# Performance work log

Measured on AMD Instinct MI355X. Metric: run time of the kernel, lower is better.

The kernel has to match this reference:

```python
import jax, jax.numpy as jnp
import numpy as np

B, H, N, D = 1, 8, 2048, 64  # n >> d: fastmax's intended long-seq / small-head-dim regime


def setup_inputs() -> dict:
    key = jax.random.key(0)
    kq, kk, kv, kr = jax.random.split(key, 4)
    q = jax.random.normal(kq, (B, H, N, D), dtype=jnp.float32)
    k = jax.random.normal(kk, (B, H, N, D), dtype=jnp.float32)
    v = jax.random.normal(kv, (B, H, N, D), dtype=jnp.float32)
    rpe_matrix = jax.random.normal(kr, (2 * N - 1, D), dtype=jnp.float32)
    return {"q": q, "k": k, "v": v, "rpe_matrix": rpe_matrix, "mask": 1}


def reference(q, k, v, rpe_matrix, mask):
    # Fastmax: 2nd-order Taylor approximation of softmax attention,
    # weight(i,j) = 1 + s_ij + s_ij^2 / 2 where s_ij = q_i . (k_j) + q_i . rpe[i-j+n-1],
    # normalized by the row-sum, optionally causal (mask).
    b, h, n, d = q.shape
    # content scores: (b,h,n,n)
    s = jnp.einsum('bhid,bhjd->bhij', q, k)
    # RPE scores: project q onto every relative-position embedding, then gather
    # the (i,j) -> i-j+n-1 diagonal structure.  qr: (b,h,n,2n-1)
    qr = jnp.einsum('bhid,md->bhim', q, rpe_matrix)
    i = jnp.arange(n)[:, None]
    j = jnp.arange(n)[None, :]
    rel = i - j + (n - 1)  # (n,n) in [0, 2n-2]
    s = s + jnp.take_along_axis(qr, rel[None, None], axis=-1)
    # Taylor-2 exp approximation
    w = 1.0 + s + 0.5 * s * s
    if mask:  # causal
        w = jnp.where(j <= i, w, 0.0)
    denom = jnp.sum(w, axis=-1, keepdims=True)  # (b,h,n,1)
    out = jnp.einsum('bhij,bhjd->bhid', w, v) / denom
    return out
```

## Files before the change

kernel.cpp:

```cpp
#include <hip/hip_runtime.h>
#include <hip/hip_bf16.h>

#define HH 8
#define NN 2048
#define DD 64

typedef __attribute__((ext_vector_type(8))) short bf16x8;
typedef __attribute__((ext_vector_type(4))) float f32x4;
typedef __attribute__((ext_vector_type(8))) unsigned short u16x8;
typedef unsigned short ushort_t;

static __device__ __forceinline__ unsigned short f2bf(float x) {
    union { float f; unsigned u; } un; un.f = x;
    unsigned r = un.u + 0x7FFFu + ((un.u >> 16) & 1u);
    return (unsigned short)(r >> 16);
}
static __device__ __forceinline__ float bf2f(unsigned short u) {
    union { unsigned u; float f; } un; un.u = ((unsigned)u) << 16;
    return un.f;
}

#define OFF_Q  0u
#define OFF_K  2097152u
#define OFF_VT 4194304u
#define OFF_R  6291456u
#define OFF_P  6815744u
#define WS_NEED (OFF_P + 256u*3u*2u*32u*68u*4u)

#define NQ4 262144
#define NR4 65520
#define CVT_BLOCKS 2305
__global__ void pre_kernel(const float* __restrict__ q, const float* __restrict__ k,
                           const float* __restrict__ r, const float* __restrict__ v,
                           ushort_t* __restrict__ ws) {
    __shared__ __align__(16) ushort_t T[64][72];
    if (blockIdx.x < CVT_BLOCKS) {
        int idx = blockIdx.x * 256 + threadIdx.x;
        const float* src; ushort_t* dst; int off;
        if (idx < NQ4) { src = q; dst = (ushort_t*)((char*)ws + OFF_Q); off = idx; }
        else if (idx < 2 * NQ4) { src = k; dst = (ushort_t*)((char*)ws + OFF_K); off = idx - NQ4; }
        else if (idx < 2 * NQ4 + NR4) { src = r; dst = (ushort_t*)((char*)ws + OFF_R); off = idx - 2 * NQ4; }
        else return;
        float4 f = *(const float4*)&src[4 * (size_t)off];
        ushort4 u; u.x = f2bf(f.x); u.y = f2bf(f.y); u.z = f2bf(f.z); u.w = f2bf(f.w);
        *(ushort4*)&dst[4 * (size_t)off] = u;
    } else {
        ushort_t* vt = (ushort_t*)((char*)ws + OFF_VT);
        const int bb = blockIdx.x - CVT_BLOCKS;
        const int h = bb >> 5;
        const int n0 = (bb & 31) * 64;
        const int tid = threadIdx.x;
        const float* vh = v + (size_t)h * NN * DD;
        #pragma unroll
        for (int p = 0; p < 4; ++p) {
            int c = tid + 256 * p; int rr = c >> 4, dc = (c & 15) << 2;
            float4 f = *(const float4*)&vh[(size_t)(n0 + rr) * DD + dc];
            T[dc + 0][rr] = f2bf(f.x); T[dc + 1][rr] = f2bf(f.y);
            T[dc + 2][rr] = f2bf(f.z); T[dc + 3][rr] = f2bf(f.w);
        }
        __syncthreads();
        #pragma unroll
        for (int p = 0; p < 2; ++p) {
            int c = tid + 256 * p; int d = c >> 3, nn = (c & 7) << 3;
            *(u16x8*)&vt[((size_t)h * 64 + d) * NN + n0 + nn] = *(const u16x8*)&T[d][nn];
        }
    }
}

__global__ __launch_bounds__(256, 3)
void fastmax_main(const ushort_t* __restrict__ wsb, float* __restrict__ wsPart)
{
    __shared__ __align__(16) ushort_t Qs[32][72];
    __shared__ __align__(16) ushort_t Ks[64][72];
    __shared__ __align__(16) ushort_t Bs[96][72];
    __shared__ __align__(16) ushort_t Vts[80][72];
    __shared__ __align__(16) unsigned char U[11776];

    ushort_t* TsP = (ushort_t*)U;
    ushort_t* WsP = (ushort_t*)(U + 6656);
    float*    Epi = (float*)U;

    const ushort_t* qb  = (const ushort_t*)((const char*)wsb + OFF_Q);
    const ushort_t* kb  = (const ushort_t*)((const char*)wsb + OFF_K);
    const ushort_t* vtb = (const ushort_t*)((const char*)wsb + OFF_VT);
    const ushort_t* rb  = (const ushort_t*)((const char*)wsb + OFF_R);

    const int tid = threadIdx.x;
    const int w   = tid >> 6;
    const int l   = tid & 63;
    const int lq  = l >> 4;
    const int ln  = l & 15;
    const int rt  = w & 1;
    const int ch  = w >> 1;

    const int stream = blockIdx.x;
    const int sub    = blockIdx.y;
    const int head   = stream & 7;
    const int p      = stream >> 3;
    const int tileA  = 63 - p;
    const int njtA   = (tileA >> 1) + 1;
    const int tileB  = p;
    const int njtB   = (p >> 1) + 1;
    const int u0     = 11 * sub, u1 = u0 + 11;

    const ushort_t* qh  = qb  + (size_t)head * NN * DD;
    const ushort_t* kh  = kb  + (size_t)head * NN * DD;
    const ushort_t* vth = vtb + (size_t)head * DD * NN;

    for (int idx = tid; idx < 16 * 72; idx += 256) {
        int r = idx / 72, c = idx - r * 72;
        Vts[64 + r][c] = (r == 0) ? (ushort_t)0x3F80 : (ushort_t)0;
    }

    const int sw = 16 * rt - 32 * ch + 32;

    #pragma unroll 1
    for (int seg = 0; seg < 2; ++seg) {
        int tile, jlo, jhi, role;
        if (seg == 0) {
            tile = tileB; role = 0;
            jlo = u0; jhi = (u1 < njtB) ? u1 : njtB;
        } else {
            tile = tileA; role = 1;
            int a0 = (u0 > njtB) ? u0 : njtB;
            jlo = a0 - njtB; jhi = u1 - njtB;
            if (jhi > njtA) jhi = njtA;
        }
        if (jlo >= jhi) continue;
        const int i0 = tile * 32;

        __syncthreads();
        { int r = tid >> 3, dc = (tid & 7) << 3;
          *(u16x8*)&Qs[r][dc] = *(const u16x8*)&qh[(size_t)(i0 + r) * DD + dc]; }
        __syncthreads();

        bf16x8 qf0 = *(const bf16x8*)&Qs[16 * rt + ln][ 0 + 8 * lq];
        bf16x8 qf1 = *(const bf16x8*)&Qs[16 * rt + ln][32 + 8 * lq];
        bf16x8 vdf = *(const bf16x8*)&Vts[64 + ln][32 * ch + 8 * lq];

        f32x4 acc0 = {0,0,0,0}, acc1 = {0,0,0,0}, acc2 = {0,0,0,0}, acc3 = {0,0,0,0};
        f32x4 accD = {0,0,0,0};

        for (int jt = jlo; jt < jhi; ++jt) {
            const int j0 = jt * 64;
            __syncthreads();

            #pragma unroll
            for (int p2 = 0; p2 < 2; ++p2) {
                int c = tid + 256 * p2; int r = c >> 3, dc = (c & 7) << 3;
                *(u16x8*)&Ks[r][dc] = *(const u16x8*)&kh[(size_t)(j0 + r) * DD + dc];
            }
            const int relbase = i0 - j0 + 1984;
            #pragma unroll
            for (int p2 = 0; p2 < 3; ++p2) {
                int c = tid + 256 * p2; int r = c >> 3, dc = (c & 7) << 3;
                int row = relbase + r; if (row > 4094) row = 4094;
                *(u16x8*)&Bs[r][dc] = *(const u16x8*)&rb[(size_t)row * DD + dc];
            }
            #pragma unroll
            for (int p2 = 0; p2 < 2; ++p2) {
                int c = tid + 256 * p2; int d = c >> 3, nc = (c & 7) << 3;
                *(u16x8*)&Vts[d][nc] = *(const u16x8*)&vth[(size_t)d * NN + j0 + nc];
            }
            __syncthreads();

            f32x4 s0 = {0,0,0,0}, s1 = {0,0,0,0};
            {
                bf16x8 b00 = *(const bf16x8*)&Ks[32 * ch      + ln][ 0 + 8 * lq];
                bf16x8 b01 = *(const bf16x8*)&Ks[32 * ch      + ln][32 + 8 * lq];
                bf16x8 b10 = *(const bf16x8*)&Ks[32 * ch + 16 + ln][ 0 + 8 * lq];
                bf16x8 b11 = *(const bf16x8*)&Ks[32 * ch + 16 + ln][32 + 8 * lq];
                s0 = __builtin_amdgcn_mfma_f32_16x16x32_bf16(qf0, b00, s0, 0, 0, 0);
                s0 = __builtin_amdgcn_mfma_f32_16x16x32_bf16(qf1, b01, s0, 0, 0, 0);
                s1 = __builtin_amdgcn_mfma_f32_16x16x32_bf16(qf0, b10, s1, 0, 0, 0);
                s1 = __builtin_amdgcn_mfma_f32_16x16x32_bf16(qf1, b11, s1, 0, 0, 0);
            }

            #pragma unroll
            for (int bt = 0; bt < 3; ++bt) {
                f32x4 t = {0,0,0,0};
                bf16x8 b0 = *(const bf16x8*)&Bs[sw + 16 * bt + ln][ 0 + 8 * lq];
                bf16x8 b1 = *(const bf16x8*)&Bs[sw + 16 * bt + ln][32 + 8 * lq];
                t = __builtin_amdgcn_mfma_f32_16x16x32_bf16(qf0, b0, t, 0, 0, 0);
                t = __builtin_amdgcn_mfma_f32_16x16x32_bf16(qf1, b1, t, 0, 0, 0);
                #pragma unroll
                for (int e = 0; e < 4; ++e)
                    TsP[(w * 16 + 4 * lq + e) * 52 + 16 * bt + ln] = f2bf(t[e]);
            }

            #pragma unroll
            for (int ct = 0; ct < 2; ++ct) {
                f32x4 sv = ct ? s1 : s0;
                #pragma unroll
                for (int e = 0; e < 4; ++e) {
                    int rp = 4 * lq + e;
                    int cp = 16 * ct + ln;
                    int bw = rp - cp + 31;
                    float s = sv[e] + bf2f(TsP[(w * 16 + rp) * 52 + bw]);
                    float wv = 1.0f + s + 0.5f * s * s;
                    if (j0 + 32 * ch + cp > i0 + 16 * rt + rp) wv = 0.0f;
                    WsP[(w * 16 + rp) * 40 + cp] = f2bf(wv);
                }
            }

            {
                bf16x8 af = *(const bf16x8*)&WsP[(w * 16 + ln) * 40 + 8 * lq];
                bf16x8 b;
                b = *(const bf16x8*)&Vts[ 0 + ln][32 * ch + 8 * lq];
                acc0 = __builtin_amdgcn_mfma_f32_16x16x32_bf16(af, b, acc0, 0, 0, 0);
                b = *(const bf16x8*)&Vts[16 + ln][32 * ch + 8 * lq];
                acc1 = __builtin_amdgcn_mfma_f32_16x16x32_bf16(af, b, acc1, 0, 0, 0);
                b = *(const bf16x8*)&Vts[32 + ln][32 * ch + 8 * lq];
                acc2 = __builtin_amdgcn_mfma_f32_16x16x32_bf16(af, b, acc2, 0, 0, 0);
                b = *(const bf16x8*)&Vts[48 + ln][32 * ch + 8 * lq];
                acc3 = __builtin_amdgcn_mfma_f32_16x16x32_bf16(af, b, acc3, 0, 0, 0);
                accD = __builtin_amdgcn_mfma_f32_16x16x32_bf16(af, vdf, accD, 0, 0, 0);
            }
        }

        __syncthreads();
        if (ch == 0) {
            #pragma unroll
            for (int e = 0; e < 4; ++e) {
                int r = 16 * rt + 4 * lq + e;
                Epi[r * 68 +  0 + ln] = acc0[e];
                Epi[r * 68 + 16 + ln] = acc1[e];
                Epi[r * 68 + 32 + ln] = acc2[e];
                Epi[r * 68 + 48 + ln] = acc3[e];
                if (ln == 0) Epi[r * 68 + 64] = accD[e];
            }
        }
        __syncthreads();
        if (ch == 1) {
            #pragma unroll
            for (int e = 0; e < 4; ++e) {
                int r = 16 * rt + 4 * lq + e;
                Epi[r * 68 +  0 + ln] += acc0[e];
                Epi[r * 68 + 16 + ln] += acc1[e];
                Epi[r * 68 + 32 + ln] += acc2[e];
                Epi[r * 68 + 48 + ln] += acc3[e];
                if (ln == 0) Epi[r * 68 + 64] += accD[e];
            }
        }
        __syncthreads();
        {
            float* dst = wsPart + ((size_t)((stream * 3 + sub) * 2 + role)) * (32 * 68);
            for (int idx = tid; idx < 32 * 68; idx += 256) dst[idx] = Epi[idx];
        }
    }
}

__global__ void combine_kernel(const float* __restrict__ wsPart, float* __restrict__ outg) {
    const int c = blockIdx.x;
    const int head = c >> 6;
    const int t = c & 63;
    const int p = (t < 63 - t) ? t : 63 - t;
    const int role = (t == p) ? 0 : 1;
    const int stream = p * 8 + head;
    const int njtB = (p >> 1) + 1;
    const float* P[3]; int nP = 0;
    #pragma unroll
    for (int s = 0; s < 3; ++s) {
        bool valid = role ? (11 * s + 11 > njtB) : (11 * s < njtB);
        if (valid) P[nP++] = wsPart + ((size_t)((stream * 3 + s) * 2 + role)) * (32 * 68);
    }
    float* oh = outg + (size_t)head * NN * DD;
    #pragma unroll
    for (int e2 = 0; e2 < 8; ++e2) {
        int idx = threadIdx.x + 256 * e2;
        int r = idx >> 6, d = idx & 63;
        float num = 0.f, den = 0.f;
        for (int s = 0; s < nP; ++s) {
            num += P[s][r * 68 + d];
            den += P[s][r * 68 + 64];
        }
        oh[(size_t)(t * 32 + r) * DD + d] = num / den;
    }
}

__global__ __launch_bounds__(256, 2)
void fastmax_fallback(const float* __restrict__ qg0, const float* __restrict__ kg0,
                      const float* __restrict__ vg0, const float* __restrict__ rg,
                      float* __restrict__ outg)
{
    __shared__ __align__(16) ushort_t Qs[32][72];
    __shared__ __align__(16) ushort_t Ks[64][72];
    __shared__ __align__(16) ushort_t Bs[96][72];
    __shared__ __align__(16) ushort_t Vts[96][72];
    __shared__ __align__(16) float    Tsf[32][97];
    __shared__ __align__(16) ushort_t Wsf[32][72];
    __shared__ float denomLds[32];

    const int tid = threadIdx.x;
    const int w = tid >> 6, l = tid & 63, lq = l >> 4, ln = l & 15;
    const int head = blockIdx.x & 7, ib = blockIdx.x >> 3;
    const int it = 63 - ib, i0 = it * 32, njt = (it >> 1) + 1;
    const float* qg = qg0 + (size_t)head * NN * DD;
    const float* kg = kg0 + (size_t)head * NN * DD;
    const float* vg = vg0 + (size_t)head * NN * DD;
    float* og = outg + (size_t)head * NN * DD;
    {
        #pragma unroll
        for (int p = 0; p < 2; ++p) {
            int c = tid + 256 * p; int r = c >> 4, dc = (c & 15) << 2;
            float4 f = *(const float4*)&qg[(size_t)(i0 + r) * DD + dc];
            ushort4 u; u.x = f2bf(f.x); u.y = f2bf(f.y); u.z = f2bf(f.z); u.w = f2bf(f.w);
            *(ushort4*)&Qs[r][dc] = u;
        }
        for (int idx = tid; idx < 32 * 72; idx += 256) {
            int rr = idx / 72, cc = idx - rr * 72;
            Vts[64 + rr][cc] = (rr == 0) ? (ushort_t)0x3F80 : (ushort_t)0;
        }
    }
    f32x4 a0 = {0,0,0,0}, a1 = {0,0,0,0}, a2 = {0,0,0,0};
    const int pr = w & 1, rt = w & 1, cp = w >> 1;
    for (int jt = 0; jt < njt; ++jt) {
        const int j0 = jt * 64;
        __syncthreads();
        #pragma unroll
        for (int p = 0; p < 4; ++p) {
            int c = tid + 256 * p; int r = c >> 4, dc = (c & 15) << 2;
            float4 f = *(const float4*)&kg[(size_t)(j0 + r) * DD + dc];
            ushort4 u; u.x = f2bf(f.x); u.y = f2bf(f.y); u.z = f2bf(f.z); u.w = f2bf(f.w);
            *(ushort4*)&Ks[r][dc] = u;
        }
        const int relbase = i0 - j0 + 1984;
        #pragma unroll
        for (int p = 0; p < 6; ++p) {
            int c = tid + 256 * p; int r = c >> 4, dc = (c & 15) << 2;
            int row = relbase + r; if (row > 4094) row = 4094;
            float4 f = *(const float4*)&rg[(size_t)row * DD + dc];
            ushort4 u; u.x = f2bf(f.x); u.y = f2bf(f.y); u.z = f2bf(f.z); u.w = f2bf(f.w);
            *(ushort4*)&Bs[r][dc] = u;
        }
        #pragma unroll
        for (int p = 0; p < 4; ++p) {
            int c = tid + 256 * p; int r = c >> 4, dc = (c & 15) << 2;
            float4 f = *(const float4*)&vg[(size_t)(j0 + r) * DD + dc];
            Vts[dc + 0][r] = f2bf(f.x); Vts[dc + 1][r] = f2bf(f.y);
            Vts[dc + 2][r] = f2bf(f.z); Vts[dc + 3][r] = f2bf(f.w);
        }
        __syncthreads();
        f32x4 s0 = {0,0,0,0}, s1 = {0,0,0,0};
        #pragma unroll
        for (int ks = 0; ks < 2; ++ks) {
            bf16x8 a = *(const bf16x8*)&Qs[16 * rt + ln][32 * ks + 8 * lq];
            bf16x8 b0 = *(const bf16x8*)&Ks[32 * cp + ln][32 * ks + 8 * lq];
            bf16x8 b1 = *(const bf16x8*)&Ks[32 * cp + 16 + ln][32 * ks + 8 * lq];
            s0 = __builtin_amdgcn_mfma_f32_16x16x32_bf16(a, b0, s0, 0, 0, 0);
            s1 = __builtin_amdgcn_mfma_f32_16x16x32_bf16(a, b1, s1, 0, 0, 0);
        }
        #pragma unroll
        for (int kk = 0; kk < 3; ++kk) {
            int bt = (w >> 1) + 2 * kk;
            f32x4 t = {0,0,0,0};
            #pragma unroll
            for (int ks = 0; ks < 2; ++ks) {
                bf16x8 a = *(const bf16x8*)&Qs[16 * rt + ln][32 * ks + 8 * lq];
                bf16x8 b = *(const bf16x8*)&Bs[16 * bt + ln][32 * ks + 8 * lq];
                t = __builtin_amdgcn_mfma_f32_16x16x32_bf16(a, b, t, 0, 0, 0);
            }
            #pragma unroll
            for (int e = 0; e < 4; ++e) Tsf[16 * rt + 4 * lq + e][16 * bt + ln] = t[e];
        }
        __syncthreads();
        #pragma unroll
        for (int ct2 = 0; ct2 < 2; ++ct2) {
            f32x4 sv = ct2 ? s1 : s0;
            int c_loc = 32 * cp + 16 * ct2 + ln, j = j0 + c_loc;
            #pragma unroll
            for (int e = 0; e < 4; ++e) {
                int r_loc = 16 * rt + 4 * lq + e, i = i0 + r_loc;
                float s = sv[e] + Tsf[r_loc][r_loc - c_loc + 63];
                float wv = 1.0f + s + 0.5f * s * s;
                if (j > i) wv = 0.0f;
                Wsf[r_loc][c_loc] = f2bf(wv);
            }
        }
        __syncthreads();
        {
            bf16x8 af0 = *(const bf16x8*)&Wsf[16 * pr + ln][ 0 + 8 * lq];
            bf16x8 af1 = *(const bf16x8*)&Wsf[16 * pr + ln][32 + 8 * lq];
            int pn0 = w >> 1; bf16x8 b;
            b = *(const bf16x8*)&Vts[16 * (pn0 + 0) + ln][ 0 + 8 * lq];
            a0 = __builtin_amdgcn_mfma_f32_16x16x32_bf16(af0, b, a0, 0, 0, 0);
            b = *(const bf16x8*)&Vts[16 * (pn0 + 0) + ln][32 + 8 * lq];
            a0 = __builtin_amdgcn_mfma_f32_16x16x32_bf16(af1, b, a0, 0, 0, 0);
            b = *(const bf16x8*)&Vts[16 * (pn0 + 2) + ln][ 0 + 8 * lq];
            a1 = __builtin_amdgcn_mfma_f32_16x16x32_bf16(af0, b, a1, 0, 0, 0);
            b = *(const bf16x8*)&Vts[16 * (pn0 + 2) + ln][32 + 8 * lq];
            a1 = __builtin_amdgcn_mfma_f32_16x16x32_bf16(af1, b, a1, 0, 0, 0);
            b = *(const bf16x8*)&Vts[16 * (pn0 + 4) + ln][ 0 + 8 * lq];
            a2 = __builtin_amdgcn_mfma_f32_16x16x32_bf16(af0, b, a2, 0, 0, 0);
            b = *(const bf16x8*)&Vts[16 * (pn0 + 4) + ln][32 + 8 * lq];
            a2 = __builtin_amdgcn_mfma_f32_16x16x32_bf16(af1, b, a2, 0, 0, 0);
        }
    }
    if (w < 2 && ln == 0) {
        #pragma unroll
        for (int e = 0; e < 4; ++e) denomLds[16 * pr + 4 * lq + e] = a2[e];
    }
    __syncthreads();
    #pragma unroll
    for (int k = 0; k < 2; ++k) {
        int pn = (w >> 1) + 2 * k;
        f32x4 acc = k ? a1 : a0;
        #pragma unroll
        for (int e = 0; e < 4; ++e) {
            int r_loc = 16 * pr + 4 * lq + e;
            og[(size_t)(i0 + r_loc) * DD + 16 * pn + ln] = acc[e] / denomLds[r_loc];
        }
    }
}

extern "C" void kernel_launch(void* const* d_in, const int* in_sizes, int n_in,
                              void* d_out, int out_size, void* d_ws, size_t ws_size,
                              hipStream_t stream) {
    const float* q   = (const float*)d_in[0];
    const float* k   = (const float*)d_in[1];
    const float* v   = (const float*)d_in[2];
    const float* rpe = (const float*)d_in[3];
    float* out = (float*)d_out;

    if (ws_size >= WS_NEED) {
        ushort_t* wsb = (ushort_t*)d_ws;
        float* wsPart = (float*)((char*)d_ws + OFF_P);
        hipLaunchKernelGGL(pre_kernel, dim3(CVT_BLOCKS + 256), dim3(256), 0, stream,
                           q, k, rpe, v, wsb);
        hipLaunchKernelGGL(fastmax_main, dim3(256, 3), dim3(256), 0, stream, wsb, wsPart);
        hipLaunchKernelGGL(combine_kernel, dim3(512), dim3(256), 0, stream, wsPart, out);
    } else {
        hipLaunchKernelGGL(fastmax_fallback, dim3(512), dim3(256), 0, stream,
                           q, k, v, rpe, out);
    }
}
```

Before: 111.8 us.

## Restructure main kernel into independent per-wave 32x32 MFMA tasks without LDS staging

Each wave now independently handles one 32-row query tile over a slice of key tiles, giving 1536 wave tasks split six ways per stream instead of three. It switches from 16x16x32 to 32x32x16 MFMA and reads K, RPE and V^T fragments directly from global memory instead of staging them through shared LDS tiles with block-wide barriers. LDS is used only per wave for the RPE diagonal gather and the weight matrix. The aim is to remove __syncthreads overhead and raise parallelism, at the cost of more global/L2 traffic, more partial results for the combine kernel to read, and larger register accumulators.

```diff
diff --git a/kernel.cpp b/kernel.cpp
--- a/kernel.cpp
+++ b/kernel.cpp
@@ -6,7 +6,7 @@
 #define DD 64
 
 typedef __attribute__((ext_vector_type(8))) short bf16x8;
-typedef __attribute__((ext_vector_type(4))) float f32x4;
+typedef __attribute__((ext_vector_type(16))) float f32x16;
 typedef __attribute__((ext_vector_type(8))) unsigned short u16x8;
 typedef unsigned short ushort_t;
 
@@ -14,10 +14,6 @@
     union { float f; unsigned u; } un; un.f = x;
     unsigned r = un.u + 0x7FFFu + ((un.u >> 16) & 1u);
     return (unsigned short)(r >> 16);
-}
-static __device__ __forceinline__ float bf2f(unsigned short u) {
-    union { unsigned u; float f; } un; un.u = ((unsigned)u) << 16;
-    return un.f;
 }
 
 #define OFF_Q  0u
@@ -25,7 +21,7 @@
 #define OFF_VT 4194304u
 #define OFF_R  6291456u
 #define OFF_P  6815744u
-#define WS_NEED (OFF_P + 256u*3u*2u*32u*68u*4u)
+#define WS_NEED (OFF_P + 1536u*2u*2080u*4u)
 
 #define NQ4 262144
 #define NR4 65520
@@ -67,18 +63,11 @@
     }
 }
 
-__global__ __launch_bounds__(256, 3)
+__global__ __launch_bounds__(128, 2)
 void fastmax_main(const ushort_t* __restrict__ wsb, float* __restrict__ wsPart)
 {
-    __shared__ __align__(16) ushort_t Qs[32][72];
-    __shared__ __align__(16) ushort_t Ks[64][72];
-    __shared__ __align__(16) ushort_t Bs[96][72];
-    __shared__ __align__(16) ushort_t Vts[80][72];
-    __shared__ __align__(16) unsigned char U[11776];
-
-    ushort_t* TsP = (ushort_t*)U;
-    ushort_t* WsP = (ushort_t*)(U + 6656);
-    float*    Epi = (float*)U;
+    __shared__ __align__(16) float    Ts[2][96 * 34];
+    __shared__ __align__(16) ushort_t Ws[2][32 * 96];
 
     const ushort_t* qb  = (const ushort_t*)((const char*)wsb + OFF_Q);
     const ushort_t* kb  = (const ushort_t*)((const char*)wsb + OFF_K);
@@ -86,183 +75,152 @@
     const ushort_t* rb  = (const ushort_t*)((const char*)wsb + OFF_R);
 
     const int tid = threadIdx.x;
-    const int w   = tid >> 6;
+    const int wv  = tid >> 6;
     const int l   = tid & 63;
-    const int lq  = l >> 4;
-    const int ln  = l & 15;
-    const int rt  = w & 1;
-    const int ch  = w >> 1;
-
-    const int stream = blockIdx.x;
-    const int sub    = blockIdx.y;
-    const int head   = stream & 7;
-    const int p      = stream >> 3;
-    const int tileA  = 63 - p;
-    const int njtA   = (tileA >> 1) + 1;
-    const int tileB  = p;
-    const int njtB   = (p >> 1) + 1;
-    const int u0     = 11 * sub, u1 = u0 + 11;
+    const int ln  = l & 31;
+    const int h2  = l >> 5;
+    float*    tsW = &Ts[wv][0];
+    ushort_t* wsW = &Ws[wv][0];
+
+    const int wtask = blockIdx.x * 2 + wv;
+    const int s     = wtask / 6;
+    const int c     = wtask - 6 * s;
+    const int head  = s & 7;
+    const int p     = s >> 3;
+    const int u0    = (33 * c + 5) / 6;
+    const int u1    = (33 * c + 38) / 6;
+    const int njtB  = (p >> 1) + 1;
 
     const ushort_t* qh  = qb  + (size_t)head * NN * DD;
     const ushort_t* kh  = kb  + (size_t)head * NN * DD;
     const ushort_t* vth = vtb + (size_t)head * DD * NN;
 
-    for (int idx = tid; idx < 16 * 72; idx += 256) {
-        int r = idx / 72, c = idx - r * 72;
-        Vts[64 + r][c] = (r == 0) ? (ushort_t)0x3F80 : (ushort_t)0;
-    }
-
-    const int sw = 16 * rt - 32 * ch + 32;
+    const short one = (ln == 0) ? (short)0x3F80 : (short)0;
+    const bf16x8 dfrag = {one, one, one, one, one, one, one, one};
 
     #pragma unroll 1
-    for (int seg = 0; seg < 2; ++seg) {
-        int tile, jlo, jhi, role;
-        if (seg == 0) {
-            tile = tileB; role = 0;
-            jlo = u0; jhi = (u1 < njtB) ? u1 : njtB;
-        } else {
-            tile = tileA; role = 1;
-            int a0 = (u0 > njtB) ? u0 : njtB;
-            jlo = a0 - njtB; jhi = u1 - njtB;
-            if (jhi > njtA) jhi = njtA;
-        }
+    for (int role = 0; role < 2; ++role) {
+        const int tile = role ? (63 - p) : p;
+        int jlo = role ? ((u0 > njtB ? u0 : njtB) - njtB) : u0;
+        int jhi = role ? (u1 - njtB) : (u1 < njtB ? u1 : njtB);
         if (jlo >= jhi) continue;
         const int i0 = tile * 32;
 
-        __syncthreads();
-        { int r = tid >> 3, dc = (tid & 7) << 3;
-          *(u16x8*)&Qs[r][dc] = *(const u16x8*)&qh[(size_t)(i0 + r) * DD + dc]; }
-        __syncthreads();
-
-        bf16x8 qf0 = *(const bf16x8*)&Qs[16 * rt + ln][ 0 + 8 * lq];
-        bf16x8 qf1 = *(const bf16x8*)&Qs[16 * rt + ln][32 + 8 * lq];
-        bf16x8 vdf = *(const bf16x8*)&Vts[64 + ln][32 * ch + 8 * lq];
-
-        f32x4 acc0 = {0,0,0,0}, acc1 = {0,0,0,0}, acc2 = {0,0,0,0}, acc3 = {0,0,0,0};
-        f32x4 accD = {0,0,0,0};
+        bf16x8 qf0 = *(const bf16x8*)&qh[(i0 + ln) * DD +  0 + 8 * h2];
+        bf16x8 qf1 = *(const bf16x8*)&qh[(i0 + ln) * DD + 16 + 8 * h2];
+        bf16x8 qf2 = *(const bf16x8*)&qh[(i0 + ln) * DD + 32 + 8 * h2];
+        bf16x8 qf3 = *(const bf16x8*)&qh[(i0 + ln) * DD + 48 + 8 * h2];
+
+        f32x16 acc0 = {0,0,0,0,0,0,0,0,0,0,0,0,0,0,0,0};
+        f32x16 acc1 = {0,0,0,0,0,0,0,0,0,0,0,0,0,0,0,0};
+        f32x16 accD = {0,0,0,0,0,0,0,0,0,0,0,0,0,0,0,0};
 
         for (int jt = jlo; jt < jhi; ++jt) {
             const int j0 = jt * 64;
-            __syncthreads();
-
-            #pragma unroll
-            for (int p2 = 0; p2 < 2; ++p2) {
-                int c = tid + 256 * p2; int r = c >> 3, dc = (c & 7) << 3;
-                *(u16x8*)&Ks[r][dc] = *(const u16x8*)&kh[(size_t)(j0 + r) * DD + dc];
-            }
             const int relbase = i0 - j0 + 1984;
-            #pragma unroll
-            for (int p2 = 0; p2 < 3; ++p2) {
-                int c = tid + 256 * p2; int r = c >> 3, dc = (c & 7) << 3;
-                int row = relbase + r; if (row > 4094) row = 4094;
-                *(u16x8*)&Bs[r][dc] = *(const u16x8*)&rb[(size_t)row * DD + dc];
-            }
-            #pragma unroll
-            for (int p2 = 0; p2 < 2; ++p2) {
-                int c = tid + 256 * p2; int d = c >> 3, nc = (c & 7) << 3;
-                *(u16x8*)&Vts[d][nc] = *(const u16x8*)&vth[(size_t)d * NN + j0 + nc];
-            }
-            __syncthreads();
-
-            f32x4 s0 = {0,0,0,0}, s1 = {0,0,0,0};
+
+            f32x16 s0 = {0,0,0,0,0,0,0,0,0,0,0,0,0,0,0,0};
+            f32x16 s1 = {0,0,0,0,0,0,0,0,0,0,0,0,0,0,0,0};
             {
-                bf16x8 b00 = *(const bf16x8*)&Ks[32 * ch      + ln][ 0 + 8 * lq];
-                bf16x8 b01 = *(const bf16x8*)&Ks[32 * ch      + ln][32 + 8 * lq];
-                bf16x8 b10 = *(const bf16x8*)&Ks[32 * ch + 16 + ln][ 0 + 8 * lq];
-                bf16x8 b11 = *(const bf16x8*)&Ks[32 * ch + 16 + ln][32 + 8 * lq];
-                s0 = __builtin_amdgcn_mfma_f32_16x16x32_bf16(qf0, b00, s0, 0, 0, 0);
-                s0 = __builtin_amdgcn_mfma_f32_16x16x32_bf16(qf1, b01, s0, 0, 0, 0);
-                s1 = __builtin_amdgcn_mfma_f32_16x16x32_bf16(qf0, b10, s1, 0, 0, 0);
-                s1 = __builtin_amdgcn_mfma_f32_16x16x32_bf16(qf1, b11, s1, 0, 0, 0);
+                const ushort_t* k0p = &kh[(j0 + ln) * DD + 8 * h2];
+                const ushort_t* k1p = &kh[(j0 + 32 + ln) * DD + 8 * h2];
+                bf16x8 b;
+                b = *(const bf16x8*)(k0p +  0); s0 = __builtin_amdgcn_mfma_f32_32x32x16_bf16(qf0, b, s0, 0, 0, 0);
+                b = *(const bf16x8*)(k0p + 16); s0 = __builtin_amdgcn_mfma_f32_32x32x16_bf16(qf1, b, s0, 0, 0, 0);
+                b = *(const bf16x8*)(k0p + 32); s0 = __builtin_amdgcn_mfma_f32_32x32x16_bf16(qf2, b, s0, 0, 0, 0);
+                b = *(const bf16x8*)(k0p + 48); s0 = __builtin_amdgcn_mfma_f32_32x32x16_bf16(qf3, b, s0, 0, 0, 0);
+                b = *(const bf16x8*)(k1p +  0); s1 = __builtin_amdgcn_mfma_f32_32x32x16_bf16(qf0, b, s1, 0, 0, 0);
+                b = *(const bf16x8*)(k1p + 16); s1 = __builtin_amdgcn_mfma_f32_32x32x16_bf16(qf1, b, s1, 0, 0, 0);
+                b = *(const bf16x8*)(k1p + 32); s1 = __builtin_amdgcn_mfma_f32_32x32x16_bf16(qf2, b, s1, 0, 0, 0);
+                b = *(const bf16x8*)(k1p + 48); s1 = __builtin_amdgcn_mfma_f32_32x32x16_bf16(qf3, b, s1, 0, 0, 0);
             }
 
             #pragma unroll
             for (int bt = 0; bt < 3; ++bt) {
-                f32x4 t = {0,0,0,0};
-                bf16x8 b0 = *(const bf16x8*)&Bs[sw + 16 * bt + ln][ 0 + 8 * lq];
-                bf16x8 b1 = *(const bf16x8*)&Bs[sw + 16 * bt + ln][32 + 8 * lq];
-                t = __builtin_amdgcn_mfma_f32_16x16x32_bf16(qf0, b0, t, 0, 0, 0);
-                t = __builtin_amdgcn_mfma_f32_16x16x32_bf16(qf1, b1, t, 0, 0, 0);
+                int row = relbase + 32 * bt + ln;
+                if (row > 4094) row = 4094;
+                const ushort_t* bp = &rb[row * DD + 8 * h2];
+                f32x16 t = {0,0,0,0,0,0,0,0,0,0,0,0,0,0,0,0};
+                bf16x8 b;
+                b = *(const bf16x8*)(bp +  0); t = __builtin_amdgcn_mfma_f32_32x32x16_bf16(qf0, b, t, 0, 0, 0);
+                b = *(const bf16x8*)(bp + 16); t = __builtin_amdgcn_mfma_f32_32x32x16_bf16(qf1, b, t, 0, 0, 0);
+                b = *(const bf16x8*)(bp + 32); t = __builtin_amdgcn_mfma_f32_32x32x16_bf16(qf2, b, t, 0, 0, 0);
+                b = *(const bf16x8*)(bp + 48); t = __builtin_amdgcn_mfma_f32_32x32x16_bf16(qf3, b, t, 0, 0, 0);
+                float* base = tsW + (32 * bt + ln) * 34 + 4 * h2;
                 #pragma unroll
-                for (int e = 0; e < 4; ++e)
-                    TsP[(w * 16 + 4 * lq + e) * 52 + 16 * bt + ln] = f2bf(t[e]);
-            }
-
-            #pragma unroll
-            for (int ct = 0; ct < 2; ++ct) {
-                f32x4 sv = ct ? s1 : s0;
+                for (int p2 = 0; p2 < 8; ++p2) {
+                    int reg = 2 * p2;
+                    int r = (reg & 3) + 8 * (reg >> 2);
+                    *(float2*)(base + r) = make_float2(t[reg], t[reg + 1]);
+                }
+            }
+
+            #pragma unroll
+            for (int nt = 0; nt < 2; ++nt) {
+                const f32x16 sv = nt ? s1 : s0;
+                const int cloc = 32 * nt + ln;
+                const int gbase = 2142 - 34 * cloc;
                 #pragma unroll
-                for (int e = 0; e < 4; ++e) {
-                    int rp = 4 * lq + e;
-                    int cp = 16 * ct + ln;
-                    int bw = rp - cp + 31;
-                    float s = sv[e] + bf2f(TsP[(w * 16 + rp) * 52 + bw]);
-                    float wv = 1.0f + s + 0.5f * s * s;
-                    if (j0 + 32 * ch + cp > i0 + 16 * rt + rp) wv = 0.0f;
-                    WsP[(w * 16 + rp) * 40 + cp] = f2bf(wv);
+                for (int reg = 0; reg < 16; ++reg) {
+                    int rp = (reg & 3) + 8 * (reg >> 2) + 4 * h2;
+                    float tv = tsW[gbase + 35 * rp];
+                    float sx = sv[reg] + tv;
+                    float wx = 1.0f + sx + 0.5f * sx * sx;
+                    if (j0 + cloc > i0 + rp) wx = 0.0f;
+                    wsW[rp * 96 + cloc] = f2bf(wx);
                 }
             }
 
             {
-                bf16x8 af = *(const bf16x8*)&WsP[(w * 16 + ln) * 40 + 8 * lq];
+                bf16x8 wf0 = *(const bf16x8*)&wsW[ln * 96 +  0 + 8 * h2];
+                bf16x8 wf1 = *(const bf16x8*)&wsW[ln * 96 + 16 + 8 * h2];
+                bf16x8 wf2 = *(const bf16x8*)&wsW[ln * 96 + 32 + 8 * h2];
+                bf16x8 wf3 = *(const bf16x8*)&wsW[ln * 96 + 48 + 8 * h2];
+                const ushort_t* v0p = &vth[(size_t)ln * NN + j0 + 8 * h2];
+                const ushort_t* v1p = &vth[(size_t)(ln + 32) * NN + j0 + 8 * h2];
                 bf16x8 b;
-                b = *(const bf16x8*)&Vts[ 0 + ln][32 * ch + 8 * lq];
-                acc0 = __builtin_amdgcn_mfma_f32_16x16x32_bf16(af, b, acc0, 0, 0, 0);
-                b = *(const bf16x8*)&Vts[16 + ln][32 * ch + 8 * lq];
-                acc1 = __builtin_amdgcn_mfma_f32_16x16x32_bf16(af, b, acc1, 0, 0, 0);
-                b = *(const bf16x8*)&Vts[32 + ln][32 * ch + 8 * lq];
-                acc2 = __builtin_amdgcn_mfma_f32_16x16x32_bf16(af, b, acc2, 0, 0, 0);
-                b = *(const bf16x8*)&Vts[48 + ln][32 * ch + 8 * lq];
-                acc3 = __builtin_amdgcn_mfma_f32_16x16x32_bf16(af, b, acc3, 0, 0, 0);
-                accD = __builtin_amdgcn_mfma_f32_16x16x32_bf16(af, vdf, accD, 0, 0, 0);
-            }
-        }
-
-        __syncthreads();
-        if (ch == 0) {
-            #pragma unroll
-            for (int e = 0; e < 4; ++e) {
-                int r = 16 * rt + 4 * lq + e;
-                Epi[r * 68 +  0 + ln] = acc0[e];
-                Epi[r * 68 + 16 + ln] = acc1[e];
-                Epi[r * 68 + 32 + ln] = acc2[e];
-                Epi[r * 68 + 48 + ln] = acc3[e];
-                if (ln == 0) Epi[r * 68 + 64] = accD[e];
-            }
-        }
-        __syncthreads();
-        if (ch == 1) {
-            #pragma unroll
-            for (int e = 0; e < 4; ++e) {
-                int r = 16 * rt + 4 * lq + e;
-                Epi[r * 68 +  0 + ln] += acc0[e];
-                Epi[r * 68 + 16 + ln] += acc1[e];
-                Epi[r * 68 + 32 + ln] += acc2[e];
-                Epi[r * 68 + 48 + ln] += acc3[e];
-                if (ln == 0) Epi[r * 68 + 64] += accD[e];
-            }
-        }
-        __syncthreads();
+                b = *(const bf16x8*)(v0p +  0); acc0 = __builtin_amdgcn_mfma_f32_32x32x16_bf16(wf0, b, acc0, 0, 0, 0);
+                b = *(const bf16x8*)(v0p + 16); acc0 = __builtin_amdgcn_mfma_f32_32x32x16_bf16(wf1, b, acc0, 0, 0, 0);
+                b = *(const bf16x8*)(v0p + 32); acc0 = __builtin_amdgcn_mfma_f32_32x32x16_bf16(wf2, b, acc0, 0, 0, 0);
+                b = *(const bf16x8*)(v0p + 48); acc0 = __builtin_amdgcn_mfma_f32_32x32x16_bf16(wf3, b, acc0, 0, 0, 0);
+                b = *(const bf16x8*)(v1p +  0); acc1 = __builtin_amdgcn_mfma_f32_32x32x16_bf16(wf0, b, acc1, 0, 0, 0);
+                b = *(const bf16x8*)(v1p + 16); acc1 = __builtin_amdgcn_mfma_f32_32x32x16_bf16(wf1, b, acc1, 0, 0, 0);
+                b = *(const bf16x8*)(v1p + 32); acc1 = __builtin_amdgcn_mfma_f32_32x32x16_bf16(wf2, b, acc1, 0, 0, 0);
+                b = *(const bf16x8*)(v1p + 48); acc1 = __builtin_amdgcn_mfma_f32_32x32x16_bf16(wf3, b, acc1, 0, 0, 0);
+                accD = __builtin_amdgcn_mfma_f32_32x32x16_bf16(wf0, dfrag, accD, 0, 0, 0);
+                accD = __builtin_amdgcn_mfma_f32_32x32x16_bf16(wf1, dfrag, accD, 0, 0, 0);
+                accD = __builtin_amdgcn_mfma_f32_32x32x16_bf16(wf2, dfrag, accD, 0, 0, 0);
+                accD = __builtin_amdgcn_mfma_f32_32x32x16_bf16(wf3, dfrag, accD, 0, 0, 0);
+            }
+        }
+
         {
-            float* dst = wsPart + ((size_t)((stream * 3 + sub) * 2 + role)) * (32 * 68);
-            for (int idx = tid; idx < 32 * 68; idx += 256) dst[idx] = Epi[idx];
+            float* dst = wsPart + ((size_t)wtask * 2 + role) * 2080;
+            #pragma unroll
+            for (int reg = 0; reg < 16; ++reg) {
+                int rr = (reg & 3) + 8 * (reg >> 2) + 4 * h2;
+                dst[rr * 65 + ln]      = acc0[reg];
+                dst[rr * 65 + 32 + ln] = acc1[reg];
+                if (ln == 0) dst[rr * 65 + 64] = accD[reg];
+            }
         }
     }
 }
 
 __global__ void combine_kernel(const float* __restrict__ wsPart, float* __restrict__ outg) {
-    const int c = blockIdx.x;
-    const int head = c >> 6;
-    const int t = c & 63;
-    const int p = (t < 63 - t) ? t : 63 - t;
+    const int blk  = blockIdx.x;
+    const int head = blk >> 6;
+    const int t    = blk & 63;
+    const int p    = (t < 63 - t) ? t : 63 - t;
     const int role = (t == p) ? 0 : 1;
-    const int stream = p * 8 + head;
+    const int s    = p * 8 + head;
     const int njtB = (p >> 1) + 1;
-    const float* P[3]; int nP = 0;
+    const float* P[6]; int nP = 0;
     #pragma unroll
-    for (int s = 0; s < 3; ++s) {
-        bool valid = role ? (11 * s + 11 > njtB) : (11 * s < njtB);
-        if (valid) P[nP++] = wsPart + ((size_t)((stream * 3 + s) * 2 + role)) * (32 * 68);
+    for (int c = 0; c < 6; ++c) {
+        int u0 = (33 * c + 5) / 6, u1 = (33 * c + 38) / 6;
+        bool valid = role ? (u1 > njtB) : (u0 < njtB);
+        if (valid) P[nP++] = wsPart + ((size_t)(s * 6 + c) * 2 + role) * 2080;
     }
     float* oh = outg + (size_t)head * NN * DD;
     #pragma unroll
@@ -270,14 +228,15 @@
         int idx = threadIdx.x + 256 * e2;
         int r = idx >> 6, d = idx & 63;
         float num = 0.f, den = 0.f;
-        for (int s = 0; s < nP; ++s) {
-            num += P[s][r * 68 + d];
-            den += P[s][r * 68 + 64];
+        for (int q2 = 0; q2 < nP; ++q2) {
+            num += P[q2][r * 65 + d];
+            den += P[q2][r * 65 + 64];
         }
         oh[(size_t)(t * 32 + r) * DD + d] = num / den;
     }
 }
 
+typedef __attribute__((ext_vector_type(4))) float f32x4;
 __global__ __launch_bounds__(256, 2)
 void fastmax_fallback(const float* __restrict__ qg0, const float* __restrict__ kg0,
                       const float* __restrict__ vg0, const float* __restrict__ rg,
@@ -427,7 +386,7 @@
         float* wsPart = (float*)((char*)d_ws + OFF_P);
         hipLaunchKernelGGL(pre_kernel, dim3(CVT_BLOCKS + 256), dim3(256), 0, stream,
                            q, k, rpe, v, wsb);
-        hipLaunchKernelGGL(fastmax_main, dim3(256, 3), dim3(256), 0, stream, wsb, wsPart);
+        hipLaunchKernelGGL(fastmax_main, dim3(768), dim3(128), 0, stream, wsb, wsPart);
         hipLaunchKernelGGL(combine_kernel, dim3(512), dim3(256), 0, stream, wsPart, out);
     } else {
         hipLaunchKernelGGL(fastmax_fallback, dim3(512), dim3(256), 0, stream,
```

Result: slower. 129.2 us (+15.5%).
